# Optimization experiments

Measured on AMD Instinct MI355X. Metric: run time of the kernel, lower is better.

The kernel has to match this reference:

```python
import jax, jax.numpy as jnp
import numpy as np

N, D_IN, D_H = 8192, 512, 512


def setup_inputs() -> dict:
    key = jax.random.key(0)
    kH, kWq, kbq, kWk, kbk = jax.random.split(key, 5)
    s_in = 1.0 / np.sqrt(D_IN)
    return {
        "H": jax.random.normal(kH, (N, D_IN), dtype=jnp.float32),
        "Wq": jax.random.normal(kWq, (D_IN, D_H), dtype=jnp.float32) * s_in,
        "bq": jax.random.normal(kbq, (D_H,), dtype=jnp.float32) * 0.01,
        "Wk": jax.random.normal(kWk, (D_IN, D_H), dtype=jnp.float32) * s_in,
        "bk": jax.random.normal(kbk, (D_H,), dtype=jnp.float32) * 0.01,
    }


def reference(H, Wq, bq, Wk, bk):
    # H: [N, T]; Q, K: [N, d_h]
    Q = H @ Wq + bq
    K = H @ Wk + bk
    # A: [N, N] raw scores
    A = Q @ K.T
    n = A.shape[0]
    # torch.where(eye, 0, A): zero out the diagonal BEFORE scale/softmax
    A = A.at[jnp.arange(n), jnp.arange(n)].set(0.0)
    A = A / jnp.sqrt(jnp.asarray(K.shape[-1], A.dtype))
    A = jax.nn.softmax(A, axis=-1)
    # aggregate values (= H itself) and add residual
    return A @ H + H
```

## Files before the change

### kernel.cpp

```cpp
#include <hip/hip_runtime.h>
#include <cstdint>
#include <cstddef>

#define GLOBAL_AS __attribute__((address_space(1)))
#define LDS_AS __attribute__((address_space(3)))

typedef __attribute__((ext_vector_type(8))) short short8;
typedef __attribute__((ext_vector_type(4))) float floatx4;
typedef __attribute__((ext_vector_type(4))) int int4v;
typedef __attribute__((ext_vector_type(8))) int int8v;

#if defined(__has_builtin)
#if __has_builtin(__builtin_amdgcn_cvt_pk_fp8_f32)
#define HAVE_HW_FP8 1
#endif
#endif

static __device__ __forceinline__ unsigned short f2bf(float f) {
  uint32_t u = __builtin_bit_cast(uint32_t, f);
  u += 0x7fffu + ((u >> 16) & 1u);
  return (unsigned short)(u >> 16);
}

static __device__ __forceinline__ unsigned char f2fp8(float f) {
#ifdef HAVE_HW_FP8
  float c = fminf(fmaxf(f, -448.f), 448.f);
  return (unsigned char)(__builtin_amdgcn_cvt_pk_fp8_f32(c, 0.f, 0, false) & 0xff);
#else
  unsigned char s = 0;
  if (f < 0.f) { s = 0x80; f = -f; }
  if (f >= 448.f) return s | 0x7e;
  if (f < 0.015625f) { int r = (int)(f * 512.f + 0.5f); return s | (unsigned char)r; }
  uint32_t u = __builtin_bit_cast(uint32_t, f);
  int e = (int)((u >> 23) & 0xff) - 127;
  uint32_t keep = (u >> 20) & 7, rest = u & 0xfffffu;
  if (rest > 0x80000u || (rest == 0x80000u && (keep & 1))) ++keep;
  if (keep == 8) { keep = 0; ++e; }
  if (e > 8) return s | 0x7e;
  return s | (unsigned char)(((e + 7) << 3) | keep);
#endif
}

static __device__ __forceinline__ uint32_t pack4fp8(const float e[4]) {
#ifdef HAVE_HW_FP8
  const uint32_t p01 = (uint32_t)__builtin_amdgcn_cvt_pk_fp8_f32(e[0], e[1], 0, false);
  const uint32_t p23 = (uint32_t)__builtin_amdgcn_cvt_pk_fp8_f32(e[2], e[3], 0, false);
  return (p01 & 0xffffu) | (p23 << 16);
#else
  return (uint32_t)f2fp8(e[0]) | ((uint32_t)f2fp8(e[1]) << 8) |
         ((uint32_t)f2fp8(e[2]) << 16) | ((uint32_t)f2fp8(e[3]) << 24);
#endif
}

static __device__ __forceinline__ uint32_t gather_dword(uint32_t w, int quad, int l15) {
  const int src = quad * 16 + 4 * (l15 & 3);
  const int sh = (l15 >> 2) * 8;
  const uint32_t v0 = (uint32_t)__shfl((int)w, src);
  const uint32_t v1 = (uint32_t)__shfl((int)w, src + 1);
  const uint32_t v2 = (uint32_t)__shfl((int)w, src + 2);
  const uint32_t v3 = (uint32_t)__shfl((int)w, src + 3);
  return ((v0 >> sh) & 0xffu) | (((v1 >> sh) & 0xffu) << 8) |
         (((v2 >> sh) & 0xffu) << 16) | (((v3 >> sh) & 0xffu) << 24);
}

static __device__ __forceinline__ void wait_vm0() {
  __builtin_amdgcn_s_waitcnt(0x0f70);
}

static __device__ __forceinline__ int8v load_frag32(const unsigned char* base, int row, int quad) {
  const int h = row & 7;
  const int c0 = (2 * quad) ^ h;
  const int c1 = (2 * quad + 1) ^ h;
  const int4v lo = *(const int4v*)(base + row * 128 + c0 * 16);
  const int4v hi = *(const int4v*)(base + row * 128 + c1 * 16);
  int8v r;
  r[0] = lo[0]; r[1] = lo[1]; r[2] = lo[2]; r[3] = lo[3];
  r[4] = hi[0]; r[5] = hi[1]; r[6] = hi[2]; r[7] = hi[3];
  return r;
}

static __device__ __forceinline__ floatx4 mx_mfma(int8v a, int8v b, floatx4 c) {
  return __builtin_amdgcn_mfma_scale_f32_16x16x128_f8f6f4(a, b, c, 0, 0, 0, 0x7f, 0, 0x7f);
}

__global__ __launch_bounds__(256) void transpose_h_kernel(
    const float* __restrict__ in, unsigned char* __restrict__ outT8,
    unsigned short* __restrict__ outN, int R, int C) {
  __shared__ float t[64][65];
  const int bc = blockIdx.x * 64;
  const int br = blockIdx.y * 64;
  const int tc = threadIdx.x & 63;
  const int tr = threadIdx.x >> 6;
  for (int r = tr; r < 64; r += 4) {
    const float v = in[(size_t)(br + r) * C + bc + tc];
    t[r][tc] = v;
    outN[(size_t)(br + r) * C + bc + tc] = f2bf(v);
  }
  __syncthreads();
  for (int r = tr; r < 64; r += 4)
    outT8[(size_t)(bc + r) * R + br + tc] = f2fp8(t[tc][r]);
}

__global__ __launch_bounds__(256) void transpose_w_kernel(
    const float* __restrict__ in, unsigned short* __restrict__ outT, int R, int C) {
  __shared__ float t[64][65];
  const int bc = blockIdx.x * 64;
  const int br = blockIdx.y * 64;
  const int tc = threadIdx.x & 63;
  const int tr = threadIdx.x >> 6;
  for (int r = tr; r < 64; r += 4)
    t[r][tc] = in[(size_t)(br + r) * C + bc + tc];
  __syncthreads();
  for (int r = tr; r < 64; r += 4)
    outT[(size_t)(bc + r) * R + br + tc] = f2bf(t[tc][r]);
}

__global__ __launch_bounds__(256) void pack_bias_kernel(
    const float* __restrict__ bq, const float* __restrict__ bk,
    float* __restrict__ bqk) {
  int i = blockIdx.x * 256 + threadIdx.x;
  bqk[i] = (i < 512) ? bq[i] : bk[i - 512];
}

__global__ __launch_bounds__(256, 4) void gemm_proj(
    const unsigned short* __restrict__ A,
    const unsigned short* __restrict__ Bt,
    int Ncols, int K,
    const float* __restrict__ bias,
    unsigned char* __restrict__ C8)
{
  __shared__ unsigned short As[2][128 * 32];
  __shared__ unsigned short Bs[2][128 * 32];

  const int tid  = threadIdx.x;
  const int lane = tid & 63;
  const int wave = tid >> 6;
  const int wr   = (wave >> 1) * 64;
  const int wc   = (wave & 1) * 64;
  const int quad = lane >> 4;
  const int l15  = lane & 15;
  const int bm   = blockIdx.y * 128;
  const int bn   = blockIdx.x * 128;

  const int c0 = tid, c1 = tid + 256;
  const int r0a = c0 >> 2, k0a = (c0 & 3) << 3;
  const int r1a = c1 >> 2, k1a = (c1 & 3) << 3;

  auto stage = [&](int kt, int b) {
    __builtin_amdgcn_global_load_lds(
        (const GLOBAL_AS void*)(A + (size_t)(bm + r0a) * K + kt + k0a),
        (LDS_AS void*)(&As[b][c0 * 8]), 16, 0, 0);
    __builtin_amdgcn_global_load_lds(
        (const GLOBAL_AS void*)(A + (size_t)(bm + r1a) * K + kt + k1a),
        (LDS_AS void*)(&As[b][c1 * 8]), 16, 0, 0);
    __builtin_amdgcn_global_load_lds(
        (const GLOBAL_AS void*)(Bt + (size_t)(bn + r0a) * K + kt + k0a),
        (LDS_AS void*)(&Bs[b][c0 * 8]), 16, 0, 0);
    __builtin_amdgcn_global_load_lds(
        (const GLOBAL_AS void*)(Bt + (size_t)(bn + r1a) * K + kt + k1a),
        (LDS_AS void*)(&Bs[b][c1 * 8]), 16, 0, 0);
  };

  floatx4 acc[4][4];
#pragma unroll
  for (int i = 0; i < 4; ++i)
#pragma unroll
    for (int j = 0; j < 4; ++j)
      acc[i][j] = (floatx4){0.f, 0.f, 0.f, 0.f};

  stage(0, 0);
  const int nIter = K >> 5;
  for (int it = 0; it < nIter; ++it) {
    const int b = it & 1;
    wait_vm0();
    __syncthreads();
    if (it + 1 < nIter) stage((it + 1) << 5, b ^ 1);

    short8 af[4], bfr[4];
#pragma unroll
    for (int i = 0; i < 4; ++i)
      af[i] = *(const short8*)(&As[b][(wr + i * 16 + l15) * 32 + quad * 8]);
#pragma unroll
    for (int j = 0; j < 4; ++j)
      bfr[j] = *(const short8*)(&Bs[b][(wc + j * 16 + l15) * 32 + quad * 8]);
#pragma unroll
    for (int i = 0; i < 4; ++i)
#pragma unroll
      for (int j = 0; j < 4; ++j)
        acc[i][j] = __builtin_amdgcn_mfma_f32_16x16x32_bf16(af[i], bfr[j], acc[i][j], 0, 0, 0);
  }

#pragma unroll
  for (int i = 0; i < 4; ++i) {
    const int rl = bm + wr + i * 16 + quad * 4;
#pragma unroll
    for (int r = 0; r < 4; ++r) {
      const int row = rl + r;
      float e[4];
#pragma unroll
      for (int j = 0; j < 4; ++j)
        e[j] = acc[i][j][r] + bias[bn + wc + j * 16 + l15];
      const uint32_t d = gather_dword(pack4fp8(e), quad, l15);
      *(uint32_t*)(C8 + (size_t)row * Ncols + bn + wc + 4 * l15) = d;
    }
  }
}

__global__ __launch_bounds__(512, 4) void gemm_qk8(
    const unsigned char* __restrict__ A,
    const unsigned char* __restrict__ Bt,
    int Ncols, int K, int lda, int ldb,
    float* __restrict__ lsum,
    int row0,
    unsigned char* __restrict__ P8)
{
  __shared__ unsigned char As[2][128 * 128];
  __shared__ unsigned char Bs[2][128 * 128];

  const int tid  = threadIdx.x;
  const int lane = tid & 63;
  const int wave = tid >> 6;
  const int wr   = (wave >> 1) * 32;
  const int wc   = (wave & 1) * 64;
  const int quad = lane >> 4;
  const int l15  = lane & 15;
  const int bm   = blockIdx.y * 128;
  const int bn   = blockIdx.x * 128;

  const int L0 = tid, L1 = tid + 512;
  const int sr0 = L0 >> 3, sc0 = ((L0 & 7) ^ (sr0 & 7)) << 4;
  const int sr1 = L1 >> 3, sc1 = ((L1 & 7) ^ (sr1 & 7)) << 4;

  auto stage = [&](int kt, int b) {
    __builtin_amdgcn_global_load_lds(
        (const GLOBAL_AS void*)(A + (size_t)(bm + sr0) * lda + kt + sc0),
        (LDS_AS void*)(&As[b][L0 * 16]), 16, 0, 0);
    __builtin_amdgcn_global_load_lds(
        (const GLOBAL_AS void*)(A + (size_t)(bm + sr1) * lda + kt + sc1),
        (LDS_AS void*)(&As[b][L1 * 16]), 16, 0, 0);
    __builtin_amdgcn_global_load_lds(
        (const GLOBAL_AS void*)(Bt + (size_t)(bn + sr0) * ldb + kt + sc0),
        (LDS_AS void*)(&Bs[b][L0 * 16]), 16, 0, 0);
    __builtin_amdgcn_global_load_lds(
        (const GLOBAL_AS void*)(Bt + (size_t)(bn + sr1) * ldb + kt + sc1),
        (LDS_AS void*)(&Bs[b][L1 * 16]), 16, 0, 0);
  };

  floatx4 acc[2][4];
#pragma unroll
  for (int i = 0; i < 2; ++i)
#pragma unroll
    for (int j = 0; j < 4; ++j)
      acc[i][j] = (floatx4){0.f, 0.f, 0.f, 0.f};

  stage(0, 0);
  const int nIter = K >> 7;
  for (int it = 0; it < nIter; ++it) {
    const int b = it & 1;
    wait_vm0();
    __syncthreads();
    if (it + 1 < nIter) stage((it + 1) << 7, b ^ 1);

    const int8v af0 = load_frag32(As[b], wr + l15, quad);
    const int8v af1 = load_frag32(As[b], wr + 16 + l15, quad);
#pragma unroll
    for (int j = 0; j < 4; ++j) {
      const int8v bf = load_frag32(Bs[b], wc + j * 16 + l15, quad);
      acc[0][j] = mx_mfma(af0, bf, acc[0][j]);
      acc[1][j] = mx_mfma(af1, bf, acc[1][j]);
    }
  }

  const float scale = 0.044194173824159216f;
#pragma unroll
  for (int i = 0; i < 2; ++i) {
    const int rl = bm + wr + i * 16 + quad * 4;
#pragma unroll
    for (int r = 0; r < 4; ++r) {
      const int row = rl + r;
      float e[4];
#pragma unroll
      for (int j = 0; j < 4; ++j) {
        const int col = bn + wc + j * 16 + l15;
        const float lg = ((row0 + row) == col) ? 0.f : acc[i][j][r] * scale;
        e[j] = fminf(__expf(lg), 448.f);
      }
      float rsum = (e[0] + e[1]) + (e[2] + e[3]);
      const uint32_t d = gather_dword(pack4fp8(e), quad, l15);
      *(uint32_t*)(P8 + (size_t)row * Ncols + bn + wc + 4 * l15) = d;
      rsum += __shfl_xor(rsum, 1);
      rsum += __shfl_xor(rsum, 2);
      rsum += __shfl_xor(rsum, 4);
      rsum += __shfl_xor(rsum, 8);
      if (l15 == 0) atomicAdd(&lsum[row0 + row], rsum);
    }
  }
}

template <bool DIRECT>
__global__ __launch_bounds__(256, 3) void gemm_pv8(
    const unsigned char* __restrict__ P,
    const unsigned char* __restrict__ Bt,
    int Kchunk,
    const float* __restrict__ lvec,
    const float* __restrict__ Hres,
    int row0,
    float* __restrict__ outp,
    size_t partStride)
{
  __shared__ unsigned char As[2][64 * 128];
  __shared__ unsigned char Bs[2][128 * 128];

  const int tid  = threadIdx.x;
  const int lane = tid & 63;
  const int wave = tid >> 6;
  const int wr   = (wave >> 1) * 32;
  const int wc   = (wave & 1) * 64;
  const int quad = lane >> 4;
  const int l15  = lane & 15;
  const int bm   = blockIdx.y * 64;
  const int bn   = blockIdx.x * 128;
  const int k0   = blockIdx.z * Kchunk;

  float* part = outp + (DIRECT ? 0 : (size_t)blockIdx.z * partStride);

  const int a0 = tid, a1 = tid + 256;
  const int ar0 = a0 >> 3, ac0 = ((a0 & 7) ^ (ar0 & 7)) << 4;
  const int ar1 = a1 >> 3, ac1 = ((a1 & 7) ^ (ar1 & 7)) << 4;
  const int b0 = tid, b1 = tid + 256, b2 = tid + 512, b3 = tid + 768;
  const int br0 = b0 >> 3, bc0 = ((b0 & 7) ^ (br0 & 7)) << 4;
  const int br1 = b1 >> 3, bc1 = ((b1 & 7) ^ (br1 & 7)) << 4;
  const int br2 = b2 >> 3, bc2 = ((b2 & 7) ^ (br2 & 7)) << 4;
  const int br3 = b3 >> 3, bc3 = ((b3 & 7) ^ (br3 & 7)) << 4;

  auto stage = [&](int kt, int b) {
    __builtin_amdgcn_global_load_lds(
        (const GLOBAL_AS void*)(P + (size_t)(bm + ar0) * 8192 + kt + ac0),
        (LDS_AS void*)(&As[b][a0 * 16]), 16, 0, 0);
    __builtin_amdgcn_global_load_lds(
        (const GLOBAL_AS void*)(P + (size_t)(bm + ar1) * 8192 + kt + ac1),
        (LDS_AS void*)(&As[b][a1 * 16]), 16, 0, 0);
    __builtin_amdgcn_global_load_lds(
        (const GLOBAL_AS void*)(Bt + (size_t)(bn + br0) * 8192 + kt + bc0),
        (LDS_AS void*)(&Bs[b][b0 * 16]), 16, 0, 0);
    __builtin_amdgcn_global_load_lds(
        (const GLOBAL_AS void*)(Bt + (size_t)(bn + br1) * 8192 + kt + bc1),
        (LDS_AS void*)(&Bs[b][b1 * 16]), 16, 0, 0);
    __builtin_amdgcn_global_load_lds(
        (const GLOBAL_AS void*)(Bt + (size_t)(bn + br2) * 8192 + kt + bc2),
        (LDS_AS void*)(&Bs[b][b2 * 16]), 16, 0, 0);
    __builtin_amdgcn_global_load_lds(
        (const GLOBAL_AS void*)(Bt + (size_t)(bn + br3) * 8192 + kt + bc3),
        (LDS_AS void*)(&Bs[b][b3 * 16]), 16, 0, 0);
  };

  floatx4 acc[2][4];
#pragma unroll
  for (int i = 0; i < 2; ++i)
#pragma unroll
    for (int j = 0; j < 4; ++j)
      acc[i][j] = (floatx4){0.f, 0.f, 0.f, 0.f};

  stage(k0, 0);
  const int nIter = Kchunk >> 7;
  for (int it = 0; it < nIter; ++it) {
    const int b = it & 1;
    wait_vm0();
    __syncthreads();
    if (it + 1 < nIter) stage(k0 + ((it + 1) << 7), b ^ 1);

    const int8v af0 = load_frag32(As[b], wr + l15, quad);
    const int8v af1 = load_frag32(As[b], wr + 16 + l15, quad);
#pragma unroll
    for (int j = 0; j < 4; ++j) {
      const int8v bf = load_frag32(Bs[b], wc + j * 16 + l15, quad);
      acc[0][j] = mx_mfma(af0, bf, acc[0][j]);
      acc[1][j] = mx_mfma(af1, bf, acc[1][j]);
    }
  }

#pragma unroll
  for (int i = 0; i < 2; ++i) {
    const int rl = bm + wr + i * 16 + quad * 4;
#pragma unroll
    for (int j = 0; j < 4; ++j) {
      const int col = bn + wc + j * 16 + l15;
#pragma unroll
      for (int r = 0; r < 4; ++r) {
        const int row = rl + r;
        const float v = acc[i][j][r];
        if (DIRECT) {
          const int grow = row0 + row;
          part[(size_t)grow * 512 + col] =
              v / lvec[grow] + Hres[(size_t)grow * 512 + col];
        } else {
          part[(size_t)row * 512 + col] = v;
        }
      }
    }
  }
}

__global__ __launch_bounds__(256) void combine_kernel(
    const float* __restrict__ parts, size_t partStride, int S,
    const float* __restrict__ lvec, const float* __restrict__ Hres,
    float* __restrict__ out, int n4) {
  int i = blockIdx.x * 256 + threadIdx.x;
  if (i >= n4) return;
  float4 a = ((const float4*)parts)[i];
  for (int s = 1; s < S; ++s) {
    const float4 b = ((const float4*)(parts + (size_t)s * partStride))[i];
    a.x += b.x; a.y += b.y; a.z += b.z; a.w += b.w;
  }
  const int row = i >> 7;
  const float inv = 1.f / lvec[row];
  const float4 h = ((const float4*)Hres)[i];
  float4 o;
  o.x = a.x * inv + h.x;
  o.y = a.y * inv + h.y;
  o.z = a.z * inv + h.z;
  o.w = a.w * inv + h.w;
  ((float4*)out)[i] = o;
}

extern "C" void kernel_launch(void* const* d_in, const int* in_sizes, int n_in,
                              void* d_out, int out_size, void* d_ws, size_t ws_size,
                              hipStream_t stream) {
  const float* H  = (const float*)d_in[0];
  const float* Wq = (const float*)d_in[1];
  const float* bq = (const float*)d_in[2];
  const float* Wk = (const float*)d_in[3];
  const float* bk = (const float*)d_in[4];
  float* out = (float*)d_out;

  const int N = 8192, D = 512;

  char* ws = (char*)d_ws;
  size_t off = 0;
  auto alloc = [&](size_t bytes) { char* p = ws + off; off += bytes; return p; };
  unsigned short* Hb   = (unsigned short*)alloc((size_t)N * D * 2);
  unsigned char*  HbT8 = (unsigned char*)alloc((size_t)D * N);
  unsigned char*  QK8  = (unsigned char*)alloc((size_t)N * 2 * D);
  unsigned short* BqkT = (unsigned short*)alloc((size_t)2 * D * D * 2);
  float* bqk = (float*)alloc((size_t)2 * D * 4);
  float* l   = (float*)alloc((size_t)N * 4);
  const size_t base = off;
  unsigned char* P8 = (unsigned char*)(ws + base);

  const size_t pBytes = (size_t)N * N;
  const size_t partBytes = (size_t)N * D * 4;
  const size_t partStride = (size_t)N * D;
  const size_t avail = (ws_size > base) ? (ws_size - base) : 0;

  int S = 0;
  if (avail >= pBytes) {
    const size_t extra = avail - pBytes;
    S = (extra >= 2 * partBytes) ? 2 : 1;
  }
  float* parts = (float*)(ws + base + pBytes);

  hipMemsetAsync(l, 0, (size_t)N * 4, stream);
  transpose_h_kernel<<<dim3(D / 64, N / 64), 256, 0, stream>>>(H, HbT8, Hb, N, D);
  transpose_w_kernel<<<dim3(D / 64, D / 64), 256, 0, stream>>>(Wq, BqkT, D, D);
  transpose_w_kernel<<<dim3(D / 64, D / 64), 256, 0, stream>>>(Wk, BqkT + (size_t)D * D, D, D);
  pack_bias_kernel<<<dim3(4), 256, 0, stream>>>(bq, bk, bqk);

  gemm_proj<<<dim3(2 * D / 128, N / 128), 256, 0, stream>>>(
      Hb, BqkT, 2 * D, D, bqk, QK8);

  if (S >= 1) {
    gemm_qk8<<<dim3(N / 128, N / 128), 512, 0, stream>>>(
        QK8, QK8 + D, N, D, 2 * D, 2 * D, l, 0, P8);
    if (S == 1) {
      gemm_pv8<true><<<dim3(D / 128, N / 64, 1), 256, 0, stream>>>(
          P8, HbT8, N, l, H, 0, out, 0);
    } else {
      gemm_pv8<false><<<dim3(D / 128, N / 64, S), 256, 0, stream>>>(
          P8, HbT8, N / S, nullptr, nullptr, 0, parts, partStride);
      combine_kernel<<<dim3((N * D / 4 + 255) / 256), 256, 0, stream>>>(
          parts, partStride, S, l, H, out, N * D / 4);
    }
  } else {
    int maxRows = (int)(avail / (size_t)N);
    maxRows &= ~127;
    if (maxRows < 128) maxRows = 128;
    for (int r0 = 0; r0 < N; r0 += maxRows) {
      int rows = N - r0;
      if (rows > maxRows) rows = maxRows;
      gemm_qk8<<<dim3(N / 128, rows / 128), 512, 0, stream>>>(
          QK8 + (size_t)r0 * 2 * D, QK8 + D, N, D, 2 * D, 2 * D, l, r0, P8);
      gemm_pv8<true><<<dim3(D / 128, rows / 64, 1), 256, 0, stream>>>(
          P8, HbT8, N, l, H, r0, out, 0);
    }
  }
}
```

Measured before the change: 269.1 us.

## Restructure QK fp8 GEMM to 4 waves with 64x64 warp tiles

```diff
diff --git a/kernel.cpp b/kernel.cpp
--- a/kernel.cpp
+++ b/kernel.cpp
@@ -7,6 +7,7 @@
 
 typedef __attribute__((ext_vector_type(8))) short short8;
 typedef __attribute__((ext_vector_type(4))) float floatx4;
+typedef __attribute__((ext_vector_type(2))) long long2v;
 typedef __attribute__((ext_vector_type(4))) int int4v;
 typedef __attribute__((ext_vector_type(8))) int int8v;
 
@@ -206,7 +207,7 @@
   }
 }
 
-__global__ __launch_bounds__(512, 4) void gemm_qk8(
+__global__ __launch_bounds__(256, 4) void gemm_qk8(
     const unsigned char* __restrict__ A,
     const unsigned char* __restrict__ Bt,
     int Ncols, int K, int lda, int ldb,
@@ -214,66 +215,72 @@
     int row0,
     unsigned char* __restrict__ P8)
 {
-  __shared__ unsigned char As[2][128 * 128];
-  __shared__ unsigned char Bs[2][128 * 128];
+  __shared__ unsigned char As[2][128 * 64];
+  __shared__ unsigned char Bs[2][128 * 64];
 
   const int tid  = threadIdx.x;
   const int lane = tid & 63;
   const int wave = tid >> 6;
-  const int wr   = (wave >> 1) * 32;
+  const int wr   = (wave >> 1) * 64;
   const int wc   = (wave & 1) * 64;
   const int quad = lane >> 4;
   const int l15  = lane & 15;
   const int bm   = blockIdx.y * 128;
   const int bn   = blockIdx.x * 128;
 
-  const int L0 = tid, L1 = tid + 512;
-  const int sr0 = L0 >> 3, sc0 = ((L0 & 7) ^ (sr0 & 7)) << 4;
-  const int sr1 = L1 >> 3, sc1 = ((L1 & 7) ^ (sr1 & 7)) << 4;
+  const int c0 = tid, c1 = tid + 256;
+  const int r0a = c0 >> 2, k0a = (c0 & 3) << 4;
+  const int r1a = c1 >> 2, k1a = (c1 & 3) << 4;
 
   auto stage = [&](int kt, int b) {
     __builtin_amdgcn_global_load_lds(
-        (const GLOBAL_AS void*)(A + (size_t)(bm + sr0) * lda + kt + sc0),
-        (LDS_AS void*)(&As[b][L0 * 16]), 16, 0, 0);
-    __builtin_amdgcn_global_load_lds(
-        (const GLOBAL_AS void*)(A + (size_t)(bm + sr1) * lda + kt + sc1),
-        (LDS_AS void*)(&As[b][L1 * 16]), 16, 0, 0);
-    __builtin_amdgcn_global_load_lds(
-        (const GLOBAL_AS void*)(Bt + (size_t)(bn + sr0) * ldb + kt + sc0),
-        (LDS_AS void*)(&Bs[b][L0 * 16]), 16, 0, 0);
-    __builtin_amdgcn_global_load_lds(
-        (const GLOBAL_AS void*)(Bt + (size_t)(bn + sr1) * ldb + kt + sc1),
-        (LDS_AS void*)(&Bs[b][L1 * 16]), 16, 0, 0);
+        (const GLOBAL_AS void*)(A + (size_t)(bm + r0a) * lda + kt + k0a),
+        (LDS_AS void*)(&As[b][c0 * 16]), 16, 0, 0);
+    __builtin_amdgcn_global_load_lds(
+        (const GLOBAL_AS void*)(A + (size_t)(bm + r1a) * lda + kt + k1a),
+        (LDS_AS void*)(&As[b][c1 * 16]), 16, 0, 0);
+    __builtin_amdgcn_global_load_lds(
+        (const GLOBAL_AS void*)(Bt + (size_t)(bn + r0a) * ldb + kt + k0a),
+        (LDS_AS void*)(&Bs[b][c0 * 16]), 16, 0, 0);
+    __builtin_amdgcn_global_load_lds(
+        (const GLOBAL_AS void*)(Bt + (size_t)(bn + r1a) * ldb + kt + k1a),
+        (LDS_AS void*)(&Bs[b][c1 * 16]), 16, 0, 0);
   };
 
-  floatx4 acc[2][4];
-#pragma unroll
-  for (int i = 0; i < 2; ++i)
+  floatx4 acc[4][4];
+#pragma unroll
+  for (int i = 0; i < 4; ++i)
 #pragma unroll
     for (int j = 0; j < 4; ++j)
       acc[i][j] = (floatx4){0.f, 0.f, 0.f, 0.f};
 
   stage(0, 0);
-  const int nIter = K >> 7;
+  const int nIter = K >> 6;
   for (int it = 0; it < nIter; ++it) {
     const int b = it & 1;
     wait_vm0();
     __syncthreads();
-    if (it + 1 < nIter) stage((it + 1) << 7, b ^ 1);
-
-    const int8v af0 = load_frag32(As[b], wr + l15, quad);
-    const int8v af1 = load_frag32(As[b], wr + 16 + l15, quad);
-#pragma unroll
-    for (int j = 0; j < 4; ++j) {
-      const int8v bf = load_frag32(Bs[b], wc + j * 16 + l15, quad);
-      acc[0][j] = mx_mfma(af0, bf, acc[0][j]);
-      acc[1][j] = mx_mfma(af1, bf, acc[1][j]);
-    }
+    if (it + 1 < nIter) stage((it + 1) << 6, b ^ 1);
+
+    long2v af[4], bfr[4];
+#pragma unroll
+    for (int i = 0; i < 4; ++i)
+      af[i] = *(const long2v*)(&As[b][(wr + i * 16 + l15) * 64 + quad * 16]);
+#pragma unroll
+    for (int j = 0; j < 4; ++j)
+      bfr[j] = *(const long2v*)(&Bs[b][(wc + j * 16 + l15) * 64 + quad * 16]);
+#pragma unroll
+    for (int i = 0; i < 4; ++i)
+#pragma unroll
+      for (int j = 0; j < 4; ++j) {
+        acc[i][j] = __builtin_amdgcn_mfma_f32_16x16x32_fp8_fp8(af[i].x, bfr[j].x, acc[i][j], 0, 0, 0);
+        acc[i][j] = __builtin_amdgcn_mfma_f32_16x16x32_fp8_fp8(af[i].y, bfr[j].y, acc[i][j], 0, 0, 0);
+      }
   }
 
   const float scale = 0.044194173824159216f;
 #pragma unroll
-  for (int i = 0; i < 2; ++i) {
+  for (int i = 0; i < 4; ++i) {
     const int rl = bm + wr + i * 16 + quad * 4;
 #pragma unroll
     for (int r = 0; r < 4; ++r) {
@@ -469,7 +476,7 @@
       Hb, BqkT, 2 * D, D, bqk, QK8);
 
   if (S >= 1) {
-    gemm_qk8<<<dim3(N / 128, N / 128), 512, 0, stream>>>(
+    gemm_qk8<<<dim3(N / 128, N / 128), 256, 0, stream>>>(
         QK8, QK8 + D, N, D, 2 * D, 2 * D, l, 0, P8);
     if (S == 1) {
       gemm_pv8<true><<<dim3(D / 128, N / 64, 1), 256, 0, stream>>>(
@@ -487,7 +494,7 @@
     for (int r0 = 0; r0 < N; r0 += maxRows) {
       int rows = N - r0;
       if (rows > maxRows) rows = maxRows;
-      gemm_qk8<<<dim3(N / 128, rows / 128), 512, 0, stream>>>(
+      gemm_qk8<<<dim3(N / 128, rows / 128), 256, 0, stream>>>(
           QK8 + (size_t)r0 * 2 * D, QK8 + D, N, D, 2 * D, 2 * D, l, r0, P8);
       gemm_pv8<true><<<dim3(D / 128, rows / 64, 1), 256, 0, stream>>>(
           P8, HbT8, N, l, H, r0, out, 0);
```

Measured after the change: 261.3 us. -2.9%, faster.
